# Kernel tuning notes

Hardware: AMD Instinct MI355X
Metric: run time of the kernel (lower is better)

Reference implementation:

```python
import jax, jax.numpy as jnp
import numpy as np

LN_EPS = 1e-5
NORM_EPS = 1e-12


def channel_layernorm(x, w, b):
    # LayerNorm over channel dim of NCHW tensor (torch permutes to NHWC; equivalent)
    mu = x.mean(axis=1, keepdims=True)
    var = x.var(axis=1, keepdims=True)
    xn = (x - mu) / jnp.sqrt(var + LN_EPS)
    return xn * w[None, :, None, None] + b[None, :, None, None]


def pconv(x, w):
    # 1x1 pointwise conv, w: (out_ch, in_ch)
    return jnp.einsum('bchw,oc->bohw', x, w)


def dwconv3(x, w):
    # depthwise 3x3, padding 1; w: (ch, 1, 3, 3)
    return jax.lax.conv_general_dilated(
        x, w, window_strides=(1, 1), padding='SAME',
        feature_group_count=x.shape[1],
        dimension_numbers=('NCHW', 'OIHW', 'NCHW'))


def l2norm(x):
    n = jnp.sqrt(jnp.sum(x * x, axis=-1, keepdims=True))
    return x / jnp.maximum(n, NORM_EPS)


def setup_inputs() -> dict:
    key = jax.random.key(0)
    ks = jax.random.split(key, 8)
    B, C, H, W = 4, 128, 128, 128
    NH, G = 8, 2

    def w(k, shape, fan_in):
        return jax.random.normal(k, shape, dtype=jnp.float32) * (fan_in ** -0.5)

    return {
        'x': jax.random.normal(ks[0], (B, C, H, W), dtype=jnp.float32),
        'ln1_w': jnp.ones((C,), jnp.float32),
        'ln1_b': jnp.zeros((C,), jnp.float32),
        'temperature': jnp.ones((NH, 1, 1), jnp.float32),
        'qkv_p_w': w(ks[1], (3 * C, C), C),
        'qkv_d_w': w(ks[2], (3 * C, 1, 3, 3), 9),
        'proj_w': w(ks[3], (C, C), C),
        'ln2_w': jnp.ones((C,), jnp.float32),
        'ln2_b': jnp.zeros((C,), jnp.float32),
        'g1_w': w(ks[4], (2 * G * C, C), C),
        'gd_w': w(ks[5], (2 * G * C, 1, 3, 3), 9),
        'g2_w': w(ks[6], (C, G * C), G * C),
        'num_heads': NH,
    }


def reference(x, ln1_w, ln1_b, temperature, qkv_p_w, qkv_d_w, proj_w,
              ln2_w, ln2_b, g1_w, gd_w, g2_w, num_heads):
    b, c, h, w_ = x.shape
    d = c // num_heads

    # --- MDTA branch ---
    y = channel_layernorm(x, ln1_w, ln1_b)
    qkv = dwconv3(pconv(y, qkv_p_w), qkv_d_w)  # (b, 3c, h, w)
    q, k, v = jnp.split(qkv, 3, axis=1)
    q = l2norm(q.reshape(b, num_heads, d, h * w_))
    k = l2norm(k.reshape(b, num_heads, d, h * w_))
    v = v.reshape(b, num_heads, d, h * w_)
    # transposed (channel) attention: (b, heads, d, d)
    attn = jnp.einsum('bhdn,bhen->bhde', q, k) * temperature[None]
    attn = jax.nn.softmax(attn, axis=-1)
    out = jnp.einsum('bhde,bhen->bhdn', attn, v).reshape(b, c, h, w_)
    x = x + pconv(out, proj_w)

    # --- GDFN branch ---
    y = channel_layernorm(x, ln2_w, ln2_b)
    hdn = dwconv3(pconv(y, g1_w), gd_w)  # (b, 2*gamma*c, h, w)
    x1, x2 = jnp.split(hdn, 2, axis=1)
    g = jax.nn.gelu(x1, approximate=False) * x2
    x = x + pconv(g, g2_w)
    return x
```

## Files before the change

### kernel.cpp

```cpp
#include <hip/hip_runtime.h>
#include <cstdint>
#include <cstddef>

typedef float f32x4 __attribute__((ext_vector_type(4)));
typedef __bf16 bf16x8 __attribute__((ext_vector_type(8)));

__device__ __forceinline__ float b2f(unsigned short u) {
    union { unsigned int i; float f; } z; z.i = ((unsigned int)u) << 16; return z.f;
}
__device__ __forceinline__ unsigned short f2b(float f) {
    union { float f; unsigned int i; } z; z.f = f;
    unsigned int x = z.i;
    return (unsigned short)((x + 0x7FFFu + ((x >> 16) & 1u)) >> 16);
}

static constexpr int C = 128;
static constexpr int NP = 16384;
static constexpr int NH = 8;

struct Ptr11 { const float* p[11]; };
__constant__ int kWN[11]   = {128, 128, 8, 49152, 3456, 16384, 128, 128, 65536, 4608, 32768};
__constant__ int kWOff[11] = {0, 128, 256, 272, 49424, 52880, 69264, 69392, 69520, 135056, 139664};
static constexpr int kWTotal = 172432;

__global__ __launch_bounds__(256)
void cvt_w_kernel(Ptr11 P, unsigned short* __restrict__ dst)
{
    int seg = blockIdx.y;
    int n = kWN[seg];
    int i = blockIdx.x * 256 + threadIdx.x;
    if (i >= n) return;
    dst[kWOff[seg] + i] = f2b(P.p[seg][i]);
}

__device__ __forceinline__ void dw8(const unsigned short* base, int y, int xi,
                                    const float* wr, float* o)
{
    uint4 rv0 = uint4{0,0,0,0}, rv1, rv2 = uint4{0,0,0,0};
    if (y > 0)   rv0 = *(const uint4*)(base - 128);
    rv1 = *(const uint4*)(base);
    if (y < 127) rv2 = *(const uint4*)(base + 128);
    uint4 rows[3] = {rv0, rv1, rv2};
    #pragma unroll
    for (int j = 0; j < 8; ++j) o[j] = 0.f;
    #pragma unroll
    for (int r = 0; r < 3; ++r) {
        union { uint4 v; unsigned short u[8]; } cv; cv.v = rows[r];
        int lh = __shfl_up((int)cv.u[7], 1, 16);
        int rh = __shfl_down((int)cv.u[0], 1, 16);
        float p[10];
        p[0] = (xi > 0)   ? b2f((unsigned short)lh) : 0.f;
        p[9] = (xi < 120) ? b2f((unsigned short)rh) : 0.f;
        #pragma unroll
        for (int j = 0; j < 8; ++j) p[j + 1] = b2f(cv.u[j]);
        #pragma unroll
        for (int j = 0; j < 8; ++j)
            o[j] += wr[r * 3] * p[j] + wr[r * 3 + 1] * p[j + 1] + wr[r * 3 + 2] * p[j + 2];
    }
}

template <int COUT>
__device__ __forceinline__ void gemm_core_tr_v(
    const unsigned short* BsT,
    unsigned short* St,
    const unsigned short* __restrict__ W,
    unsigned short* __restrict__ OutB,
    int n0, int tid)
{
    const int lane = tid & 63;
    const int wid  = tid >> 6;
    const int ln16 = lane & 15, quad = lane >> 4;
    const int wy = wid >> 1, wx = wid & 1;
    const char* bs = (const char*)BsT;
    const int swz = (ln16 & 7) << 4;
    int rbase[4];
    #pragma unroll
    for (int nt = 0; nt < 4; ++nt) {
        int n = wx * 64 + nt * 16 + ln16;
        rbase[nt] = n * 256 + quad * 16;
    }

    for (int cc = 0; cc < COUT / 128; ++cc) {
        const int m0 = cc * 128;
        f32x4 acc[4][4];
        #pragma unroll
        for (int i = 0; i < 4; ++i)
            #pragma unroll
            for (int j = 0; j < 4; ++j) acc[i][j] = f32x4{0.f, 0.f, 0.f, 0.f};

        #pragma unroll
        for (int k0 = 0; k0 < 128; k0 += 32) {
            bf16x8 afr[4], bfr[4];
            #pragma unroll
            for (int mt = 0; mt < 4; ++mt) {
                int m = m0 + wy * 64 + mt * 16 + ln16;
                uint4 v = *(const uint4*)(W + (size_t)m * 128 + k0 + quad * 8);
                afr[mt] = *(bf16x8*)&v;
            }
            #pragma unroll
            for (int nt = 0; nt < 4; ++nt) {
                uint4 v = *(const uint4*)(bs + ((rbase[nt] + k0 * 2) ^ swz));
                bfr[nt] = *(bf16x8*)&v;
            }
            #pragma unroll
            for (int mt = 0; mt < 4; ++mt)
                #pragma unroll
                for (int nt = 0; nt < 4; ++nt)
                    acc[mt][nt] = __builtin_amdgcn_mfma_f32_16x16x32_bf16(
                        afr[mt], bfr[nt], acc[mt][nt], 0, 0, 0);
        }
        #pragma unroll
        for (int h = 0; h < 2; ++h) {
            if (wy == h) {
                #pragma unroll
                for (int mt = 0; mt < 4; ++mt) {
                    int lr0 = mt * 16 + quad * 4;
                    #pragma unroll
                    for (int nt = 0; nt < 4; ++nt) {
                        int nn = wx * 64 + nt * 16 + ln16;
                        #pragma unroll
                        for (int r = 0; r < 4; ++r)
                            St[(lr0 + r) * 136 + nn] = f2b(acc[mt][nt][r]);
                    }
                }
            }
            __syncthreads();
            #pragma unroll
            for (int i = 0; i < 4; ++i) {
                int flat = tid + i * 256;
                int row = flat >> 4;
                int g = flat & 15;
                uint4 v = *(const uint4*)(&St[row * 136 + g * 8]);
                *(uint4*)(&OutB[(size_t)(m0 + h * 64 + row) * NP + n0 + g * 8]) = v;
            }
            __syncthreads();
        }
    }
}

template <int COUT>
__global__ __launch_bounds__(256)
void lngemm_kernel(const float* __restrict__ x,
                   const unsigned short* __restrict__ lg,
                   const unsigned short* __restrict__ lb,
                   const unsigned short* __restrict__ W,
                   unsigned short* __restrict__ Out)
{
    __shared__ unsigned short BsT[128 * 128];
    __shared__ float SS[4352];
    float (*Ssum)[128] = (float(*)[128])SS;
    float (*Ssq)[128]  = (float(*)[128])(SS + 1024);
    float* Mu = SS + 2048;
    float* Rs = SS + 2176;
    unsigned short* St = (unsigned short*)SS;

    const int tid = threadIdx.x;
    const int b = blockIdx.y;
    const int n0 = blockIdx.x * 128;
    const int pxg = tid & 31;
    const int cseg = tid >> 5;
    const float* xb = x + (size_t)b * C * NP + n0 + pxg * 4;

    f32x4 hv[16];
    f32x4 vs = f32x4{0.f, 0.f, 0.f, 0.f}, vq = f32x4{0.f, 0.f, 0.f, 0.f};
    #pragma unroll
    for (int i = 0; i < 16; ++i) {
        f32x4 v = *(const f32x4*)(xb + (size_t)(cseg * 16 + i) * NP);
        hv[i] = v; vs += v; vq += v * v;
    }
    #pragma unroll
    for (int j = 0; j < 4; ++j) {
        Ssum[cseg][pxg * 4 + j] = vs[j];
        Ssq[cseg][pxg * 4 + j]  = vq[j];
    }
    __syncthreads();
    if (tid < 128) {
        float s = 0.f, q = 0.f;
        #pragma unroll
        for (int e = 0; e < 8; ++e) { s += Ssum[e][tid]; q += Ssq[e][tid]; }
        float mu = s * (1.f / 128.f);
        float var = q * (1.f / 128.f) - mu * mu;
        Mu[tid] = mu;
        Rs[tid] = rsqrtf(fmaxf(var, 0.f) + 1e-5f);
    }
    __syncthreads();
    f32x4 mu4 = *(const f32x4*)(&Mu[pxg * 4]);
    f32x4 rs4 = *(const f32x4*)(&Rs[pxg * 4]);

    float gwv[16], bwv[16];
    #pragma unroll
    for (int i = 0; i < 16; ++i) {
        gwv[i] = b2f(lg[cseg * 16 + i]);
        bwv[i] = b2f(lb[cseg * 16 + i]);
    }

    char* p = (char*)BsT;
    #pragma unroll
    for (int j = 0; j < 4; ++j) {
        int n = pxg * 4 + j;
        union { uint4 v[2]; unsigned short u[16]; } o;
        #pragma unroll
        for (int i = 0; i < 16; ++i)
            o.u[i] = f2b((hv[i][j] - mu4[j]) * rs4[j] * gwv[i] + bwv[i]);
        int base = n * 256 + cseg * 32;
        int sw = (n & 7) << 4;
        *(uint4*)(p + (base ^ sw))        = o.v[0];
        *(uint4*)(p + ((base + 16) ^ sw)) = o.v[1];
    }
    __syncthreads();
    gemm_core_tr_v<COUT>(BsT, St, W, Out + (size_t)b * COUT * NP, n0, tid);
}

template <int COUT>
__global__ __launch_bounds__(256)
void lngemm2_kernel(const unsigned short* __restrict__ xm,
                    const unsigned short* __restrict__ lg,
                    const unsigned short* __restrict__ lb,
                    const unsigned short* __restrict__ W,
                    unsigned short* __restrict__ Out)
{
    __shared__ unsigned short BsT[128 * 128];
    __shared__ unsigned short St[64 * 136];
    __shared__ float LSum[4][128], LSq[4][128], Mu[128], Rs[128];
    const int tid = threadIdx.x;
    const int b = blockIdx.y;
    const int n0 = blockIdx.x * 128;
    const int pxg = tid & 15;
    const int cseg = tid >> 4;
    const int lane = tid & 63;
    const unsigned short* xb = xm + (size_t)b * C * NP + n0 + pxg * 8;

    union { uint4 v; unsigned short u[8]; } hv[8];
    float s[8], q[8];
    #pragma unroll
    for (int j = 0; j < 8; ++j) { s[j] = 0.f; q[j] = 0.f; }
    #pragma unroll
    for (int i = 0; i < 8; ++i) {
        hv[i].v = *(const uint4*)(xb + (size_t)(cseg * 8 + i) * NP);
        #pragma unroll
        for (int j = 0; j < 8; ++j) {
            float v = b2f(hv[i].u[j]);
            s[j] += v; q[j] += v * v;
        }
    }
    #pragma unroll
    for (int j = 0; j < 8; ++j) {
        s[j] += __shfl_xor(s[j], 16, 64); q[j] += __shfl_xor(q[j], 16, 64);
        s[j] += __shfl_xor(s[j], 32, 64); q[j] += __shfl_xor(q[j], 32, 64);
    }
    if (lane < 16) {
        int wv = tid >> 6;
        #pragma unroll
        for (int j = 0; j < 8; ++j) {
            LSum[wv][pxg * 8 + j] = s[j];
            LSq[wv][pxg * 8 + j]  = q[j];
        }
    }
    __syncthreads();
    if (tid < 128) {
        float ss = LSum[0][tid] + LSum[1][tid] + LSum[2][tid] + LSum[3][tid];
        float qq = LSq[0][tid] + LSq[1][tid] + LSq[2][tid] + LSq[3][tid];
        float mu = ss * (1.f / 128.f);
        float var = qq * (1.f / 128.f) - mu * mu;
        Mu[tid] = mu; Rs[tid] = rsqrtf(fmaxf(var, 0.f) + 1e-5f);
    }
    __syncthreads();

    float gwv[8], bwv[8];
    #pragma unroll
    for (int i = 0; i < 8; ++i) {
        gwv[i] = b2f(lg[cseg * 8 + i]);
        bwv[i] = b2f(lb[cseg * 8 + i]);
    }
    char* p = (char*)BsT;
    #pragma unroll
    for (int j = 0; j < 8; ++j) {
        int n = pxg * 8 + j;
        float mu = Mu[n], rs = Rs[n];
        union { uint4 v; unsigned short u[8]; } o;
        #pragma unroll
        for (int i = 0; i < 8; ++i)
            o.u[i] = f2b((b2f(hv[i].u[j]) - mu) * rs * gwv[i] + bwv[i]);
        *(uint4*)(p + ((n * 256 + cseg * 16) ^ ((n & 7) << 4))) = o.v;
    }
    __syncthreads();
    gemm_core_tr_v<COUT>(BsT, St, W, Out + (size_t)b * COUT * NP, n0, tid);
}

__global__ __launch_bounds__(256)
void dwqkgram_kernel(const unsigned short* __restrict__ big,
                     const unsigned short* __restrict__ w9,
                     float* __restrict__ Spart,
                     float* __restrict__ Npart)
{
    __shared__ unsigned short qs_[16 * 520];
    __shared__ unsigned short ks_[16 * 520];
    __shared__ float Sred[4][256];
    const int h = blockIdx.x, b = blockIdx.y, sp = blockIdx.z;
    const int tid = threadIdx.x;
    const int wid = tid >> 6, lane = tid & 63;
    const int xi = (tid & 15) * 8;
    const int yr = (tid >> 4) & 3;
    const int y  = sp * 4 + yr;
    const int bh = b * NH + h;
    float* Np = Npart + ((size_t)bh * 32 + sp) * 32;

    #pragma unroll
    for (int p = 0; p < 4; ++p) {
        int qc = p * 4 + wid;
        #pragma unroll
        for (int s = 0; s < 2; ++s) {
            int ch = s * 128 + h * 16 + qc;
            const unsigned short* base = big + ((size_t)b * 384 + ch) * NP + y * 128 + xi;
            float wr[9];
            #pragma unroll
            for (int i = 0; i < 9; ++i) wr[i] = b2f(w9[ch * 9 + i]);
            float o[8];
            dw8(base, y, xi, wr, o);
            union { uint4 v; unsigned short u[8]; } res;
            float ss = 0.f;
            #pragma unroll
            for (int j = 0; j < 8; ++j) {
                res.u[j] = f2b(o[j]);
                float vv = b2f(res.u[j]);
                ss += vv * vv;
            }
            unsigned short* tile = s ? ks_ : qs_;
            *(uint4*)(&tile[qc * 520 + yr * 128 + xi]) = res.v;
            #pragma unroll
            for (int od = 32; od > 0; od >>= 1) ss += __shfl_xor(ss, od, 64);
            if (lane == 0) Np[s * 16 + qc] = ss;
        }
    }
    __syncthreads();

    const int ln16 = lane & 15, quad = lane >> 4;
    f32x4 acc = f32x4{0.f, 0.f, 0.f, 0.f};
    #pragma unroll
    for (int i = 0; i < 4; ++i) {
        int off = wid * 128 + i * 32 + quad * 8;
        uint4 qv = *(const uint4*)(&qs_[ln16 * 520 + off]);
        uint4 kv = *(const uint4*)(&ks_[ln16 * 520 + off]);
        acc = __builtin_amdgcn_mfma_f32_16x16x32_bf16(*(bf16x8*)&qv, *(bf16x8*)&kv, acc, 0, 0, 0);
    }
    #pragma unroll
    for (int r = 0; r < 4; ++r) Sred[wid][(quad * 4 + r) * 16 + ln16] = acc[r];
    __syncthreads();
    float ssum = Sred[0][tid] + Sred[1][tid] + Sred[2][tid] + Sred[3][tid];
    Spart[((size_t)bh * 32 + sp) * 256 + tid] = ssum;
}

__global__ __launch_bounds__(256)
void softwp_kernel(const float* __restrict__ Spart, const float* __restrict__ Npart,
                   const unsigned short* __restrict__ temp,
                   const unsigned short* __restrict__ proj,
                   unsigned short* __restrict__ W2)
{
    __shared__ float Ps[256];
    int bh = blockIdx.x;
    int b = bh >> 3, h = bh & 7;
    int t = threadIdx.x;
    int dq = t >> 4, dk = t & 15;
    float sacc = 0.f;
    const float* Sp = Spart + (size_t)bh * 32 * 256;
    #pragma unroll
    for (int j = 0; j < 32; ++j) sacc += Sp[j * 256 + t];
    const float* Np = Npart + (size_t)bh * 32 * 32;
    float sq = 0.f, sk = 0.f;
    #pragma unroll
    for (int sp = 0; sp < 32; ++sp) { sq += Np[sp * 32 + dq]; sk += Np[sp * 32 + 16 + dk]; }
    float nq = fmaxf(sqrtf(sq), 1e-12f);
    float nk = fmaxf(sqrtf(sk), 1e-12f);
    float v = sacc / (nq * nk) * b2f(temp[h]);
    float m = v;
    #pragma unroll
    for (int o = 8; o > 0; o >>= 1) m = fmaxf(m, __shfl_xor(m, o, 16));
    float e = __expf(v - m);
    float s = e;
    #pragma unroll
    for (int o = 8; o > 0; o >>= 1) s += __shfl_xor(s, o, 16);
    Ps[t] = e / s;
    __syncthreads();

    int co = t >> 1;
    int eo = (t & 1) * 8;
    union { uint4 v[2]; unsigned short u[16]; } pw;
    pw.v[0] = *(const uint4*)(proj + (size_t)co * 128 + h * 16);
    pw.v[1] = *(const uint4*)(proj + (size_t)co * 128 + h * 16 + 8);
    float prw[16];
    #pragma unroll
    for (int d = 0; d < 16; ++d) prw[d] = b2f(pw.u[d]);
    union { uint4 v; unsigned short u[8]; } o8;
    #pragma unroll
    for (int j = 0; j < 8; ++j) {
        int ee = eo + j;
        float s2 = 0.f;
        #pragma unroll
        for (int d = 0; d < 16; ++d) s2 += prw[d] * Ps[d * 16 + ee];
        o8.u[j] = f2b(s2);
    }
    *(uint4*)(W2 + ((size_t)b * 128 + co) * 128 + h * 16 + eo) = o8.v;
}

__global__ __launch_bounds__(256)
void projln_kernel(const unsigned short* __restrict__ W2,
                   const unsigned short* __restrict__ big,
                   const unsigned short* __restrict__ w9,
                   const float* __restrict__ Res,
                   unsigned short* __restrict__ Xmid)
{
    __shared__ unsigned short Bs[128][130];
    float* Stf = (float*)Bs;
    const int tid = threadIdx.x;
    const int b = blockIdx.y;
    const int y = blockIdx.x;
    const int n0 = y * 128;
    const unsigned short* Wb = W2 + (size_t)b * 16384;

    {
        const int xi = (tid & 15) * 8;
        const int crow = tid >> 4;
        #pragma unroll
        for (int p = 0; p < 8; ++p) {
            int c = p * 16 + crow;
            int ch = 256 + c;
            const unsigned short* base = big + ((size_t)b * 384 + ch) * NP + n0 + xi;
            float wr[9];
            #pragma unroll
            for (int i = 0; i < 9; ++i) wr[i] = b2f(w9[ch * 9 + i]);
            float o[8];
            dw8(base, y, xi, wr, o);
            union { uint4 v; unsigned int d[4]; unsigned short u[8]; } res;
            #pragma unroll
            for (int j = 0; j < 8; ++j) res.u[j] = f2b(o[j]);
            unsigned int* d = (unsigned int*)&Bs[c][xi];
            d[0] = res.d[0]; d[1] = res.d[1]; d[2] = res.d[2]; d[3] = res.d[3];
        }
    }
    __syncthreads();

    const int lane = tid & 63, wid = tid >> 6;
    const int ln16 = lane & 15, quad = lane >> 4;
    const int wy = wid >> 1, wx = wid & 1;

    f32x4 acc[4][4];
    #pragma unroll
    for (int i = 0; i < 4; ++i)
        #pragma unroll
        for (int j = 0; j < 4; ++j) acc[i][j] = f32x4{0.f, 0.f, 0.f, 0.f};

    #pragma unroll
    for (int k0 = 0; k0 < 128; k0 += 32) {
        bf16x8 afr[4], bfr[4];
        #pragma unroll
        for (int mt = 0; mt < 4; ++mt) {
            int m = wy * 64 + mt * 16 + ln16;
            uint4 v = *(const uint4*)(Wb + (size_t)m * 128 + k0 + quad * 8);
            afr[mt] = *(bf16x8*)&v;
        }
        #pragma unroll
        for (int nt = 0; nt < 4; ++nt) {
            int n = wx * 64 + nt * 16 + ln16;
            union { bf16x8 v; unsigned short u[8]; } tmp;
            #pragma unroll
            for (int j = 0; j < 8; ++j) tmp.u[j] = Bs[k0 + quad * 8 + j][n];
            bfr[nt] = tmp.v;
        }
        #pragma unroll
        for (int mt = 0; mt < 4; ++mt)
            #pragma unroll
            for (int nt = 0; nt < 4; ++nt)
                acc[mt][nt] = __builtin_amdgcn_mfma_f32_16x16x32_bf16(
                    afr[mt], bfr[nt], acc[mt][nt], 0, 0, 0);
    }
    __syncthreads();

    size_t base = (size_t)b * 128 * NP;
    #pragma unroll
    for (int mt = 0; mt < 4; ++mt) {
        int lr = wy * 16 + quad * 4;
        #pragma unroll
        for (int nt = 0; nt < 4; ++nt) {
            int nn = wx * 64 + nt * 16 + ln16;
            #pragma unroll
            for (int r = 0; r < 4; ++r)
                Stf[(lr + r) * 132 + nn] = acc[mt][nt][r];
        }
        __syncthreads();
        #pragma unroll
        for (int i = 0; i < 4; ++i) {
            int flat = tid + i * 256;
            int row = flat >> 5;
            int g = flat & 31;
            f32x4 v = *(const f32x4*)(&Stf[row * 132 + g * 4]);
            int absrow = (row >> 4) * 64 + mt * 16 + (row & 15);
            size_t idx = base + (size_t)absrow * NP + n0 + g * 4;
            f32x4 rv = *(const f32x4*)(Res + idx);
            union { uint2 v2; unsigned short u[4]; } o;
            #pragma unroll
            for (int k = 0; k < 4; ++k) o.u[k] = f2b(rv[k] + v[k]);
            *(uint2*)(Xmid + idx) = o.v2;
        }
        __syncthreads();
    }
}

template <int K>
__global__ __launch_bounds__(256)
void gemm_pconv(const unsigned short* __restrict__ W,
                const unsigned short* __restrict__ X,
                float* __restrict__ Out,
                const unsigned short* __restrict__ Res,
                int Cout)
{
    __shared__ unsigned short Bs[32][130];
    __shared__ float Stf[32 * 132];
    const int tid = threadIdx.x;
    const int b = blockIdx.z;
    const int n0 = blockIdx.x * 128;
    const int m0 = blockIdx.y * 128;
    const unsigned short* Xb = X + (size_t)b * K * NP;
    const int wid = tid >> 6;
    const int lane = tid & 63;
    const int ln16 = lane & 15;
    const int quad = lane >> 4;
    const int wy = wid >> 1;
    const int wx = wid & 1;

    f32x4 acc[4][4];
    #pragma unroll
    for (int i = 0; i < 4; ++i)
        #pragma unroll
        for (int j = 0; j < 4; ++j)
            acc[i][j] = f32x4{0.f, 0.f, 0.f, 0.f};

    for (int k0 = 0; k0 < K; k0 += 32) {
        #pragma unroll
        for (int r = 0; r < 2; ++r) {
            int flat = tid + r * 256;
            int kk = flat >> 4;
            int nn = (flat & 15) * 8;
            uint4 v = *(const uint4*)(Xb + (size_t)(k0 + kk) * NP + n0 + nn);
            unsigned int* d = (unsigned int*)&Bs[kk][nn];
            d[0] = v.x; d[1] = v.y; d[2] = v.z; d[3] = v.w;
        }
        __syncthreads();

        bf16x8 afr[4];
        #pragma unroll
        for (int mt = 0; mt < 4; ++mt) {
            int m = m0 + wy * 64 + mt * 16 + ln16;
            uint4 v = *(const uint4*)(W + (size_t)m * K + k0 + quad * 8);
            afr[mt] = *(bf16x8*)&v;
        }
        bf16x8 bfr[4];
        #pragma unroll
        for (int nt = 0; nt < 4; ++nt) {
            int n = wx * 64 + nt * 16 + ln16;
            union { bf16x8 v; unsigned short u[8]; } tmp;
            #pragma unroll
            for (int j = 0; j < 8; ++j) tmp.u[j] = Bs[quad * 8 + j][n];
            bfr[nt] = tmp.v;
        }
        #pragma unroll
        for (int mt = 0; mt < 4; ++mt)
            #pragma unroll
            for (int nt = 0; nt < 4; ++nt)
                acc[mt][nt] = __builtin_amdgcn_mfma_f32_16x16x32_bf16(
                    afr[mt], bfr[nt], acc[mt][nt], 0, 0, 0);
        __syncthreads();
    }

    size_t outbase = (size_t)b * Cout * NP;
    #pragma unroll
    for (int mt = 0; mt < 4; ++mt) {
        int lr = wy * 16 + quad * 4;
        #pragma unroll
        for (int nt = 0; nt < 4; ++nt) {
            int nn = wx * 64 + nt * 16 + ln16;
            #pragma unroll
            for (int r = 0; r < 4; ++r)
                Stf[(lr + r) * 132 + nn] = acc[mt][nt][r];
        }
        __syncthreads();
        #pragma unroll
        for (int i = 0; i < 4; ++i) {
            int flat = tid + i * 256;
            int row = flat >> 5;
            int g = flat & 31;
            f32x4 v = *(const f32x4*)(&Stf[row * 132 + g * 4]);
            int absrow = m0 + (row >> 4) * 64 + mt * 16 + (row & 15);
            size_t idx = outbase + (size_t)absrow * NP + n0 + g * 4;
            union { uint2 u2; unsigned short u[4]; } rv;
            rv.u2 = *(const uint2*)(Res + idx);
            f32x4 o;
            #pragma unroll
            for (int k = 0; k < 4; ++k) o[k] = b2f(rv.u[k]) + v[k];
            *(f32x4*)(Out + idx) = o;
        }
        __syncthreads();
    }
}

__global__ __launch_bounds__(256)
void dwgelu_kernel(const unsigned short* __restrict__ hdn,
                   const unsigned short* __restrict__ w9,
                   unsigned short* __restrict__ g)
{
    int t = blockIdx.x * 256 + threadIdx.x;
    int xi = (t & 15) * 8;
    int y  = (t >> 4) & 127;
    int bc = t >> 11;
    int c  = bc & 255;
    int b  = bc >> 8;
    const unsigned short* base1 = hdn + ((size_t)b * 512 + c) * NP + y * 128 + xi;
    const unsigned short* base2 = base1 + (size_t)256 * NP;

    float w1[9], w2[9];
    #pragma unroll
    for (int i = 0; i < 9; ++i) {
        w1[i] = b2f(w9[c * 9 + i]);
        w2[i] = b2f(w9[(c + 256) * 9 + i]);
    }

    float a1[8], a2[8];
    dw8(base1, y, xi, w1, a1);
    dw8(base2, y, xi, w2, a2);

    union { uint4 v; unsigned short u[8]; } res;
    #pragma unroll
    for (int j = 0; j < 8; ++j) {
        float u = a1[j];
        float tt = u * (0.7978845608f + 0.0356774081f * u * u);
        float e = __expf(2.f * tt);
        float th = 1.f - 2.f / (e + 1.f);
        float ge = 0.5f * u * (1.f + th);
        res.u[j] = f2b(ge * a2[j]);
    }
    *(uint4*)(g + (size_t)bc * NP + y * 128 + xi) = res.v;
}

struct Bufs {
    unsigned short* xmid;
    unsigned short* big;
    unsigned short* mid;
    float* Spart;
    float* Npart;
    unsigned short* W2;
};

static void run_pipeline(const float* x_f32, float* out_f32,
                         const unsigned short* w,
                         const Bufs& B, int nb, hipStream_t stream)
{
    const unsigned short* ln1_w   = w + 0;
    const unsigned short* ln1_b   = w + 128;
    const unsigned short* temp    = w + 256;
    const unsigned short* qkv_p_w = w + 272;
    const unsigned short* qkv_d_w = w + 49424;
    const unsigned short* proj_w  = w + 52880;
    const unsigned short* ln2_w   = w + 69264;
    const unsigned short* ln2_b   = w + 69392;
    const unsigned short* g1_w    = w + 69520;
    const unsigned short* gd_w    = w + 135056;
    const unsigned short* g2_w    = w + 139664;

    lngemm_kernel<384><<<dim3(NP / 128, nb), 256, 0, stream>>>(x_f32, ln1_w, ln1_b, qkv_p_w, B.big);
    dwqkgram_kernel<<<dim3(NH, nb, 32), 256, 0, stream>>>(B.big, qkv_d_w, B.Spart, B.Npart);
    softwp_kernel<<<nb * NH, 256, 0, stream>>>(B.Spart, B.Npart, temp, proj_w, B.W2);
    projln_kernel<<<dim3(NP / 128, nb), 256, 0, stream>>>(B.W2, B.big, qkv_d_w, x_f32, B.xmid);

    lngemm2_kernel<512><<<dim3(NP / 128, nb), 256, 0, stream>>>(B.xmid, ln2_w, ln2_b, g1_w, B.big);
    dwgelu_kernel<<<nb * 256 * NP / 2048, 256, 0, stream>>>(B.big, gd_w, B.mid);
    gemm_pconv<256><<<dim3(NP / 128, 1, nb), 256, 0, stream>>>(g2_w, B.mid, out_f32, B.xmid, 128);
}

extern "C" void kernel_launch(void* const* d_in, const int* in_sizes, int n_in,
                              void* d_out, int out_size, void* d_ws, size_t ws_size,
                              hipStream_t stream)
{
    (void)in_sizes; (void)n_in; (void)out_size;
    const float* x = (const float*)d_in[0];
    char* ws = (char*)d_ws;

    size_t off = 0;
    unsigned short* wpack = (unsigned short*)(ws + off);
    off += (size_t)kWTotal * 2;
    off = (off + 255) & ~(size_t)255;
    size_t header = off;

    auto layout = [&](int nb, size_t o, Bufs& B) -> size_t {
        B.xmid = (unsigned short*)(ws + o);  o += (size_t)nb * C * NP * 2;
        B.big  = (unsigned short*)(ws + o);  o += (size_t)nb * 512 * NP * 2;
        B.mid  = (unsigned short*)(ws + o);  o += (size_t)nb * 256 * NP * 2;
        B.Spart = (float*)(ws + o);          o += (size_t)nb * NH * 32 * 256 * 4;
        B.Npart = (float*)(ws + o);          o += (size_t)nb * NH * 32 * 32 * 4;
        B.W2   = (unsigned short*)(ws + o);  o += (size_t)nb * 128 * 128 * 2;
        return o;
    };

    Ptr11 P;
    for (int i = 0; i < 11; ++i) P.p[i] = (const float*)d_in[i + 1];
    cvt_w_kernel<<<dim3(256, 11), 256, 0, stream>>>(P, wpack);

    Bufs Bfull;
    size_t need_full = layout(4, header, Bfull);

    if (ws_size >= need_full) {
        run_pipeline(x, (float*)d_out, wpack, Bfull, 4, stream);
    } else {
        Bufs B1;
        layout(1, header, B1);
        for (int b = 0; b < 4; ++b) {
            run_pipeline(x + (size_t)b * C * NP,
                         (float*)d_out + (size_t)b * C * NP,
                         wpack, B1, 1, stream);
        }
    }
}
```

Before: 237.5 us.

## Fuse depthwise conv + GELU gating into final GDFN pointwise GEMM

Replaces the separate dwgelu kernel and the final 256→128 pointwise GEMM with one kernel. Each block computes the depthwise 3x3 conv and GELU gate for a 64-pixel row segment across all 256 channels into shared memory, then runs the MFMA GEMM straight from LDS and adds the residual. This removes the write and re-read of the 256-channel intermediate and one launch. In exchange the tiles are smaller (64 pixels), more LDS is used, halo pixels need extra scalar loads, and each block reloads the full weight matrix.

```diff
diff --git a/kernel.cpp b/kernel.cpp
--- a/kernel.cpp
+++ b/kernel.cpp
@@ -51,6 +51,39 @@
         float p[10];
         p[0] = (xi > 0)   ? b2f((unsigned short)lh) : 0.f;
         p[9] = (xi < 120) ? b2f((unsigned short)rh) : 0.f;
+        #pragma unroll
+        for (int j = 0; j < 8; ++j) p[j + 1] = b2f(cv.u[j]);
+        #pragma unroll
+        for (int j = 0; j < 8; ++j)
+            o[j] += wr[r * 3] * p[j] + wr[r * 3 + 1] * p[j + 1] + wr[r * 3 + 2] * p[j + 2];
+    }
+}
+
+__device__ __forceinline__ void dw8b(const unsigned short* base, int y, int gxi,
+                                     const float* wr, float* o)
+{
+    #pragma unroll
+    for (int j = 0; j < 8; ++j) o[j] = 0.f;
+    const int lx = gxi & 63;
+    #pragma unroll
+    for (int r = 0; r < 3; ++r) {
+        int yy = y + r - 1;
+        bool valid = (yy >= 0) && (yy <= 127);
+        const unsigned short* rp = base + (r - 1) * 128;
+        uint4 rv = uint4{0,0,0,0};
+        if (valid) rv = *(const uint4*)rp;
+        union { uint4 v; unsigned short u[8]; } cv; cv.v = rv;
+        int lh = __shfl_up((int)cv.u[7], 1, 8);
+        int rh = __shfl_down((int)cv.u[0], 1, 8);
+        float pl, pr;
+        if (gxi == 0)        pl = 0.f;
+        else if (lx == 0)    pl = valid ? b2f(rp[-1]) : 0.f;
+        else                 pl = b2f((unsigned short)lh);
+        if (gxi == 120)      pr = 0.f;
+        else if (lx == 56)   pr = valid ? b2f(rp[8]) : 0.f;
+        else                 pr = b2f((unsigned short)rh);
+        float p[10];
+        p[0] = pl; p[9] = pr;
         #pragma unroll
         for (int j = 0; j < 8; ++j) p[j + 1] = b2f(cv.u[j]);
         #pragma unroll
@@ -505,91 +538,110 @@
     }
 }
 
-template <int K>
 __global__ __launch_bounds__(256)
-void gemm_pconv(const unsigned short* __restrict__ W,
-                const unsigned short* __restrict__ X,
-                float* __restrict__ Out,
-                const unsigned short* __restrict__ Res,
-                int Cout)
-{
-    __shared__ unsigned short Bs[32][130];
-    __shared__ float Stf[32 * 132];
+void gdfn2_kernel(const unsigned short* __restrict__ W,
+                  const unsigned short* __restrict__ hdn,
+                  const unsigned short* __restrict__ w9,
+                  float* __restrict__ Out,
+                  const unsigned short* __restrict__ Res)
+{
+    __shared__ unsigned short Gs[256 * 66];
+    float* Stf = (float*)Gs;
     const int tid = threadIdx.x;
-    const int b = blockIdx.z;
-    const int n0 = blockIdx.x * 128;
-    const int m0 = blockIdx.y * 128;
-    const unsigned short* Xb = X + (size_t)b * K * NP;
-    const int wid = tid >> 6;
-    const int lane = tid & 63;
-    const int ln16 = lane & 15;
-    const int quad = lane >> 4;
-    const int wy = wid >> 1;
-    const int wx = wid & 1;
-
-    f32x4 acc[4][4];
+    const int b = blockIdx.y;
+    const int n0 = blockIdx.x * 64;
+    const int y = n0 >> 7;
+    const int x0 = n0 & 127;
+
+    {
+        const int xi = (tid & 7) * 8;
+        const int gxi = x0 + xi;
+        const int crow = tid >> 3;
+        #pragma unroll
+        for (int p = 0; p < 8; ++p) {
+            int c = p * 32 + crow;
+            const unsigned short* b1 = hdn + ((size_t)b * 512 + c) * NP + y * 128 + gxi;
+            const unsigned short* b2 = b1 + (size_t)256 * NP;
+            float w1[9], w2[9];
+            #pragma unroll
+            for (int i = 0; i < 9; ++i) {
+                w1[i] = b2f(w9[c * 9 + i]);
+                w2[i] = b2f(w9[(c + 256) * 9 + i]);
+            }
+            float a1[8], a2[8];
+            dw8b(b1, y, gxi, w1, a1);
+            dw8b(b2, y, gxi, w2, a2);
+            union { uint4 v; unsigned int d[4]; unsigned short u[8]; } res;
+            #pragma unroll
+            for (int j = 0; j < 8; ++j) {
+                float u = a1[j];
+                float tt = u * (0.7978845608f + 0.0356774081f * u * u);
+                float e = __expf(2.f * tt);
+                float th = 1.f - 2.f / (e + 1.f);
+                float ge = 0.5f * u * (1.f + th);
+                res.u[j] = f2b(ge * a2[j]);
+            }
+            unsigned int* d = (unsigned int*)&Gs[c * 66 + xi];
+            d[0] = res.d[0]; d[1] = res.d[1]; d[2] = res.d[2]; d[3] = res.d[3];
+        }
+    }
+    __syncthreads();
+
+    const int lane = tid & 63, wid = tid >> 6;
+    const int ln16 = lane & 15, quad = lane >> 4;
+    const int wy = wid >> 1, wx = wid & 1;
+
+    f32x4 acc[4][2];
     #pragma unroll
     for (int i = 0; i < 4; ++i)
         #pragma unroll
-        for (int j = 0; j < 4; ++j)
-            acc[i][j] = f32x4{0.f, 0.f, 0.f, 0.f};
-
-    for (int k0 = 0; k0 < K; k0 += 32) {
-        #pragma unroll
-        for (int r = 0; r < 2; ++r) {
-            int flat = tid + r * 256;
-            int kk = flat >> 4;
-            int nn = (flat & 15) * 8;
-            uint4 v = *(const uint4*)(Xb + (size_t)(k0 + kk) * NP + n0 + nn);
-            unsigned int* d = (unsigned int*)&Bs[kk][nn];
-            d[0] = v.x; d[1] = v.y; d[2] = v.z; d[3] = v.w;
-        }
-        __syncthreads();
-
-        bf16x8 afr[4];
+        for (int j = 0; j < 2; ++j) acc[i][j] = f32x4{0.f, 0.f, 0.f, 0.f};
+
+    #pragma unroll
+    for (int k0 = 0; k0 < 256; k0 += 32) {
+        bf16x8 afr[4], bfr[2];
         #pragma unroll
         for (int mt = 0; mt < 4; ++mt) {
-            int m = m0 + wy * 64 + mt * 16 + ln16;
-            uint4 v = *(const uint4*)(W + (size_t)m * K + k0 + quad * 8);
+            int m = wy * 64 + mt * 16 + ln16;
+            uint4 v = *(const uint4*)(W + (size_t)m * 256 + k0 + quad * 8);
             afr[mt] = *(bf16x8*)&v;
         }
-        bf16x8 bfr[4];
-        #pragma unroll
-        for (int nt = 0; nt < 4; ++nt) {
-            int n = wx * 64 + nt * 16 + ln16;
+        #pragma unroll
+        for (int nt = 0; nt < 2; ++nt) {
+            int n = wx * 32 + nt * 16 + ln16;
             union { bf16x8 v; unsigned short u[8]; } tmp;
             #pragma unroll
-            for (int j = 0; j < 8; ++j) tmp.u[j] = Bs[quad * 8 + j][n];
+            for (int j = 0; j < 8; ++j) tmp.u[j] = Gs[(k0 + quad * 8 + j) * 66 + n];
             bfr[nt] = tmp.v;
         }
         #pragma unroll
         for (int mt = 0; mt < 4; ++mt)
             #pragma unroll
-            for (int nt = 0; nt < 4; ++nt)
+            for (int nt = 0; nt < 2; ++nt)
                 acc[mt][nt] = __builtin_amdgcn_mfma_f32_16x16x32_bf16(
                     afr[mt], bfr[nt], acc[mt][nt], 0, 0, 0);
-        __syncthreads();
-    }
-
-    size_t outbase = (size_t)b * Cout * NP;
+    }
+    __syncthreads();
+
+    size_t outbase = (size_t)b * 128 * NP;
     #pragma unroll
     for (int mt = 0; mt < 4; ++mt) {
         int lr = wy * 16 + quad * 4;
         #pragma unroll
-        for (int nt = 0; nt < 4; ++nt) {
-            int nn = wx * 64 + nt * 16 + ln16;
+        for (int nt = 0; nt < 2; ++nt) {
+            int nn = wx * 32 + nt * 16 + ln16;
             #pragma unroll
             for (int r = 0; r < 4; ++r)
-                Stf[(lr + r) * 132 + nn] = acc[mt][nt][r];
+                Stf[(lr + r) * 68 + nn] = acc[mt][nt][r];
         }
         __syncthreads();
         #pragma unroll
-        for (int i = 0; i < 4; ++i) {
+        for (int i = 0; i < 2; ++i) {
             int flat = tid + i * 256;
-            int row = flat >> 5;
-            int g = flat & 31;
-            f32x4 v = *(const f32x4*)(&Stf[row * 132 + g * 4]);
-            int absrow = m0 + (row >> 4) * 64 + mt * 16 + (row & 15);
+            int row = flat >> 4;
+            int g = flat & 15;
+            f32x4 v = *(const f32x4*)(&Stf[row * 68 + g * 4]);
+            int absrow = (row >> 4) * 64 + mt * 16 + (row & 15);
             size_t idx = outbase + (size_t)absrow * NP + n0 + g * 4;
             union { uint2 u2; unsigned short u[4]; } rv;
             rv.u2 = *(const uint2*)(Res + idx);
@@ -602,48 +654,9 @@
     }
 }
 
-__global__ __launch_bounds__(256)
-void dwgelu_kernel(const unsigned short* __restrict__ hdn,
-                   const unsigned short* __restrict__ w9,
-                   unsigned short* __restrict__ g)
-{
-    int t = blockIdx.x * 256 + threadIdx.x;
-    int xi = (t & 15) * 8;
-    int y  = (t >> 4) & 127;
-    int bc = t >> 11;
-    int c  = bc & 255;
-    int b  = bc >> 8;
-    const unsigned short* base1 = hdn + ((size_t)b * 512 + c) * NP + y * 128 + xi;
-    const unsigned short* base2 = base1 + (size_t)256 * NP;
-
-    float w1[9], w2[9];
-    #pragma unroll
-    for (int i = 0; i < 9; ++i) {
-        w1[i] = b2f(w9[c * 9 + i]);
-        w2[i] = b2f(w9[(c + 256) * 9 + i]);
-    }
-
-    float a1[8], a2[8];
-    dw8(base1, y, xi, w1, a1);
-    dw8(base2, y, xi, w2, a2);
-
-    union { uint4 v; unsigned short u[8]; } res;
-    #pragma unroll
-    for (int j = 0; j < 8; ++j) {
-        float u = a1[j];
-        float tt = u * (0.7978845608f + 0.0356774081f * u * u);
-        float e = __expf(2.f * tt);
-        float th = 1.f - 2.f / (e + 1.f);
-        float ge = 0.5f * u * (1.f + th);
-        res.u[j] = f2b(ge * a2[j]);
-    }
-    *(uint4*)(g + (size_t)bc * NP + y * 128 + xi) = res.v;
-}
-
 struct Bufs {
     unsigned short* xmid;
     unsigned short* big;
-    unsigned short* mid;
     float* Spart;
     float* Npart;
     unsigned short* W2;
@@ -671,8 +684,7 @@
     projln_kernel<<<dim3(NP / 128, nb), 256, 0, stream>>>(B.W2, B.big, qkv_d_w, x_f32, B.xmid);
 
     lngemm2_kernel<512><<<dim3(NP / 128, nb), 256, 0, stream>>>(B.xmid, ln2_w, ln2_b, g1_w, B.big);
-    dwgelu_kernel<<<nb * 256 * NP / 2048, 256, 0, stream>>>(B.big, gd_w, B.mid);
-    gemm_pconv<256><<<dim3(NP / 128, 1, nb), 256, 0, stream>>>(g2_w, B.mid, out_f32, B.xmid, 128);
+    gdfn2_kernel<<<dim3(NP / 64, nb), 256, 0, stream>>>(g2_w, B.big, gd_w, out_f32, B.xmid);
 }
 
 extern "C" void kernel_launch(void* const* d_in, const int* in_sizes, int n_in,
@@ -692,7 +704,6 @@
     auto layout = [&](int nb, size_t o, Bufs& B) -> size_t {
         B.xmid = (unsigned short*)(ws + o);  o += (size_t)nb * C * NP * 2;
         B.big  = (unsigned short*)(ws + o);  o += (size_t)nb * 512 * NP * 2;
-        B.mid  = (unsigned short*)(ws + o);  o += (size_t)nb * 256 * NP * 2;
         B.Spart = (float*)(ws + o);          o += (size_t)nb * NH * 32 * 256 * 4;
         B.Npart = (float*)(ws + o);          o += (size_t)nb * NH * 32 * 32 * 4;
         B.W2   = (unsigned short*)(ws + o);  o += (size_t)nb * 128 * 128 * 2;
```

New measurement: 295.4 us. 1.24x slower.
